# Kernel optimization log

Hardware: AMD Instinct MI355X
Metric: run time of the kernel (lower is better)

The kernel has to match this reference:

```python
import jax, jax.numpy as jnp
import numpy as np

N, G, E, H, Z = 50000, 2000, 800000, 512, 64
BN_EPS = 1e-5


def setup_inputs() -> dict:
    key = jax.random.key(0)
    ks = jax.random.split(key, 10)
    x = jax.random.normal(ks[0], (N, G), dtype=jnp.float32)
    edge_index = jax.random.randint(ks[1], (2, E), 0, N, dtype=jnp.int32)
    s1 = 1.0 / np.sqrt(G)
    s2 = 1.0 / np.sqrt(H)
    return {
        "x": x,
        "edge_index": edge_index,
        "W1l": jax.random.normal(ks[2], (G, H), dtype=jnp.float32) * s1,
        "b1": jnp.zeros((H,), jnp.float32),
        "W1r": jax.random.normal(ks[3], (G, H), dtype=jnp.float32) * s1,
        "bn_gamma": jax.random.uniform(ks[4], (H,), dtype=jnp.float32) + 0.5,
        "bn_beta": jax.random.normal(ks[5], (H,), dtype=jnp.float32) * 0.1,
        "bn_mean": jax.random.normal(ks[6], (H,), dtype=jnp.float32) * 0.1,
        "bn_var": jax.random.uniform(ks[7], (H,), dtype=jnp.float32) + 0.5,
        "W2l": jax.random.normal(ks[8], (H, Z), dtype=jnp.float32) * s2,
        "b2": jnp.zeros((Z,), jnp.float32),
        "W2r": jax.random.normal(ks[9], (H, Z), dtype=jnp.float32) * s2,
    }


def _sage_conv(h, src, dst, Wl, bl, Wr, n_nodes):
    # mean aggregation of source features at destination nodes
    msg = h[src]  # [E, D] gather
    agg = jax.ops.segment_sum(msg, dst, num_segments=n_nodes)
    cnt = jax.ops.segment_sum(jnp.ones((src.shape[0],), h.dtype), dst, num_segments=n_nodes)
    agg = agg / jnp.maximum(cnt, 1.0)[:, None]
    # PyG SAGEConv: lin_l(agg) + lin_r(x), bias only on lin_l
    return agg @ Wl + bl + h @ Wr


def reference(x, edge_index, W1l, b1, W1r, bn_gamma, bn_beta, bn_mean, bn_var, W2l, b2, W2r):
    src, dst = edge_index[0], edge_index[1]
    n = x.shape[0]
    h = _sage_conv(x, src, dst, W1l, b1, W1r, n)  # [N, H]
    # BatchNorm1d (eval mode: running stats) + ReLU; dropout is identity at inference
    h = (h - bn_mean) * (bn_gamma / jnp.sqrt(bn_var + BN_EPS)) + bn_beta
    h = jax.nn.relu(h)
    z = _sage_conv(h, src, dst, W2l, b2, W2r, n)  # [N, Z]
    return z
```

## Files before the change

kernel.cpp:

```cpp
#include <hip/hip_runtime.h>


#define BN_EPS 1e-5f
#define GK 2000
#define KP 2048
#define NKT 32
#define NT2 16

typedef __attribute__((ext_vector_type(8))) short bf16x8;
typedef __attribute__((ext_vector_type(4))) float f32x4;
typedef unsigned short u16x8 __attribute__((ext_vector_type(8)));

__device__ inline unsigned short f2bf(float f) {
    union { float f; unsigned u; } v; v.f = f;
    unsigned r = (v.u + 0x7fffu + ((v.u >> 16) & 1u)) >> 16;
    return (unsigned short)r;
}
__device__ inline float bf2f(unsigned short u) {
    union { unsigned u; float f; } v; v.u = ((unsigned)u) << 16;
    return v.f;
}

#define GLL16(gp, lp) __builtin_amdgcn_global_load_lds( \
    (const __attribute__((address_space(1))) void*)(gp), \
    (__attribute__((address_space(3))) void*)(lp), 16, 0, 0)

__global__ __launch_bounds__(256) void prep_fused(
    const float* __restrict__ W1l, const float* __restrict__ W1r,
    const float* __restrict__ gamma, const float* __restrict__ beta,
    const float* __restrict__ mean, const float* __restrict__ var,
    const float* __restrict__ b1, unsigned short* __restrict__ BT,
    const float* __restrict__ W2l, const float* __restrict__ W2r,
    unsigned short* __restrict__ BT2, float* __restrict__ b1p,
    const int* __restrict__ ei, int* __restrict__ cnt, int E)
{
    const int bb = blockIdx.x;
    if (bb < 1024) {
        int idx = bb * 256 + threadIdx.x;
        int c  = idx >> 8;
        int k0 = (idx & 255) << 3;
        int cc = (c < 512) ? c : c - 512;
        float scv = gamma[cc] * rsqrtf(var[cc] + BN_EPS);
        const float* W = (c < 512) ? (W1l + cc) : (W1r + cc);
        unsigned short us[8];
#pragma unroll
        for (int j = 0; j < 8; ++j) {
            int k = k0 + j;
            float v = (k < GK) ? W[(size_t)k * 512] * scv : 0.0f;
            us[j] = f2bf(v);
        }
        *(u16x8*)&BT[(size_t)c * KP + k0] = *(u16x8*)us;
    } else if (bb < 1056) {
        int idx = (bb - 1024) * 256 + threadIdx.x;
        int c  = idx >> 6;
        int k0 = (idx & 63) << 3;
        const float* W = (c < 64) ? (W2l + c) : (W2r + (c - 64));
        unsigned short us[8];
#pragma unroll
        for (int j = 0; j < 8; ++j) us[j] = f2bf(W[(size_t)(k0 + j) * 64]);
        *(u16x8*)&BT2[(size_t)c * 512 + k0] = *(u16x8*)us;
    } else if (bb == 1056) {
#pragma unroll
        for (int h = 0; h < 2; ++h) {
            int c = threadIdx.x + h * 256;
            float scv = gamma[c] * rsqrtf(var[c] + BN_EPS);
            b1p[c] = b1[c] * scv + (beta[c] - mean[c] * scv);
        }
    } else {
        for (int i = (bb - 1057) * 256 + threadIdx.x; i < E; i += 1024 * 256)
            atomicAdd(&cnt[ei[E + i]], 1);
    }
}

__global__ __launch_bounds__(1024) void scan_kernel(const int* __restrict__ cnt,
                                                    int* __restrict__ row_start, int n) {
    __shared__ int part[1024];
    int t = threadIdx.x;
    int chunk = (n + 1023) >> 10;
    int lo = t * chunk;
    int hi = lo + chunk; if (hi > n) hi = n;
    int s = 0;
    for (int i = lo; i < hi; ++i) s += cnt[i];
    part[t] = s;
    __syncthreads();
    for (int off = 1; off < 1024; off <<= 1) {
        int add = (t >= off) ? part[t - off] : 0;
        __syncthreads();
        part[t] += add;
        __syncthreads();
    }
    int run = (t == 0) ? 0 : part[t - 1];
    for (int i = lo; i < hi; ++i) { row_start[i] = run; run += cnt[i]; }
    if (t == 1023) row_start[n] = part[1023];
}

__global__ __launch_bounds__(256) void convfill_kernel(
    const float* __restrict__ x, unsigned short* __restrict__ xb, int N,
    const int* __restrict__ ei, int E, const int* __restrict__ row_start,
    int* __restrict__ cnt, int* __restrict__ colidx)
{
    const int bb = blockIdx.x;
    if (bb < 2048) {
        const int total8 = N * 256;
        for (int idx = bb * 256 + threadIdx.x; idx < total8; idx += 2048 * 256) {
            int row = idx >> 8;
            int k8  = idx & 255;
            unsigned short us[8];
            if (k8 < 250) {
                const float4* p = (const float4*)(x + (size_t)row * 2000 + k8 * 8);
                float4 v0 = p[0], v1 = p[1];
                us[0]=f2bf(v0.x); us[1]=f2bf(v0.y); us[2]=f2bf(v0.z); us[3]=f2bf(v0.w);
                us[4]=f2bf(v1.x); us[5]=f2bf(v1.y); us[6]=f2bf(v1.z); us[7]=f2bf(v1.w);
            } else {
#pragma unroll
                for (int j = 0; j < 8; ++j) us[j] = 0;
            }
            *(u16x8*)&xb[(size_t)row * 2048 + k8 * 8] = *(u16x8*)us;
        }
    } else {
        int i = (bb - 2048) * 256 + threadIdx.x;
        if (i < E) {
            int d = ei[E + i];
            int p = atomicSub(&cnt[d], 1) - 1;
            colidx[row_start[d] + p] = ei[i];
        }
    }
}

__global__ __launch_bounds__(512) void gemm1_256(
    const unsigned short* __restrict__ xb, int M,
    const unsigned short* __restrict__ BT,
    unsigned short* __restrict__ Y)
{
    __shared__ __align__(16) unsigned short As[2][16384];
    __shared__ __align__(16) unsigned short Bs[2][16384];

    const int t = threadIdx.x, wid = t >> 6, lane = t & 63;
    const int nbr = (M + 255) >> 8;
    const int nwg = nbr * 4;
    const int b   = blockIdx.x;
    int swz = ((nwg & 7) == 0) ? (b & 7) * (nwg >> 3) + (b >> 3) : b;
    const int row0 = (swz >> 2) << 8;
    const int col0 = (swz & 3) << 8;

    const unsigned short* aSrc[4];
    const unsigned short* bSrc[4];
#pragma unroll
    for (int j = 0; j < 4; ++j) {
        int c = t + 512 * j;
        int l = (c & 7) ^ ((c >> 3) & 7);
        int rA = row0 + (c >> 3); if (rA >= M) rA = M - 1;
        aSrc[j] = xb + (size_t)rA * KP + l * 8;
        bSrc[j] = BT + (size_t)(col0 + (c >> 3)) * KP + l * 8;
    }

#define STG_HA0(kt, buf) do { \
        GLL16(aSrc[0] + (size_t)(kt) * 64, &As[buf][(size_t)t * 8]); \
        GLL16(aSrc[1] + (size_t)(kt) * 64, &As[buf][(size_t)(t + 512) * 8]); } while (0)
#define STG_HA1(kt, buf) do { \
        GLL16(aSrc[2] + (size_t)(kt) * 64, &As[buf][(size_t)(1024 + t) * 8]); \
        GLL16(aSrc[3] + (size_t)(kt) * 64, &As[buf][(size_t)(1536 + t) * 8]); } while (0)
#define STG_HB0(kt, buf) do { \
        GLL16(bSrc[0] + (size_t)(kt) * 64, &Bs[buf][(size_t)t * 8]); \
        GLL16(bSrc[1] + (size_t)(kt) * 64, &Bs[buf][(size_t)(t + 512) * 8]); } while (0)
#define STG_HB1(kt, buf) do { \
        GLL16(bSrc[2] + (size_t)(kt) * 64, &Bs[buf][(size_t)(1024 + t) * 8]); \
        GLL16(bSrc[3] + (size_t)(kt) * 64, &Bs[buf][(size_t)(1536 + t) * 8]); } while (0)

    const int wr = wid >> 2, wc = wid & 3;
    const int fr16 = lane & 15;
    const int j4  = lane >> 4;
    const int sl7 = fr16 & 7;
    const int sA0 = ((j4    ) ^ sl7) << 4;
    const int sA1 = ((4 + j4) ^ sl7) << 4;
    const int rbA = (wr * 128 + fr16) << 7;
    const int rbB = (wc * 64  + fr16) << 7;

    f32x4 acc[8][4];
#pragma unroll
    for (int m = 0; m < 8; ++m)
#pragma unroll
        for (int n = 0; n < 4; ++n) acc[m][n] = (f32x4)0.0f;

    STG_HB0(0, 0); STG_HA0(0, 0); STG_HA1(0, 0); STG_HB1(0, 0);
    STG_HB0(1, 1); STG_HA0(1, 1); STG_HA1(1, 1);
    asm volatile("s_waitcnt vmcnt(6)" ::: "memory");
    __builtin_amdgcn_s_barrier();
    __builtin_amdgcn_sched_barrier(0);

    for (int tk = 0; tk < NKT; ++tk) {
        const int buf = tk & 1, obuf = buf ^ 1;
        const char* Ab = (const char*)&As[buf][0];
        const char* Bb = (const char*)&Bs[buf][0];
        bf16x8 af[4][2], bfA[2][2], bfB[2][2];

#pragma unroll
        for (int m = 0; m < 4; ++m) {
            af[m][0] = *(const bf16x8*)(Ab + rbA + (m << 11) + sA0);
            af[m][1] = *(const bf16x8*)(Ab + rbA + (m << 11) + sA1);
        }
#pragma unroll
        for (int n = 0; n < 2; ++n) {
            bfA[n][0] = *(const bf16x8*)(Bb + rbB + (n << 11) + sA0);
            bfA[n][1] = *(const bf16x8*)(Bb + rbB + (n << 11) + sA1);
        }
        STG_HB1(tk + 1, obuf);
        __builtin_amdgcn_s_barrier();
        __builtin_amdgcn_sched_barrier(0);
        __builtin_amdgcn_s_setprio(1);
#pragma unroll
        for (int m = 0; m < 4; ++m)
#pragma unroll
            for (int n = 0; n < 2; ++n) {
                acc[m][n] = __builtin_amdgcn_mfma_f32_16x16x32_bf16(
                    af[m][0], bfA[n][0], acc[m][n], 0, 0, 0);
                acc[m][n] = __builtin_amdgcn_mfma_f32_16x16x32_bf16(
                    af[m][1], bfA[n][1], acc[m][n], 0, 0, 0);
            }
        __builtin_amdgcn_s_setprio(0);

#pragma unroll
        for (int n = 0; n < 2; ++n) {
            bfB[n][0] = *(const bf16x8*)(Bb + rbB + ((n + 2) << 11) + sA0);
            bfB[n][1] = *(const bf16x8*)(Bb + rbB + ((n + 2) << 11) + sA1);
        }
        asm volatile("s_waitcnt lgkmcnt(0)" ::: "memory");
        __builtin_amdgcn_s_barrier();
        __builtin_amdgcn_sched_barrier(0);
        __builtin_amdgcn_s_setprio(1);
#pragma unroll
        for (int m = 0; m < 4; ++m)
#pragma unroll
            for (int n = 0; n < 2; ++n) {
                acc[m][n + 2] = __builtin_amdgcn_mfma_f32_16x16x32_bf16(
                    af[m][0], bfB[n][0], acc[m][n + 2], 0, 0, 0);
                acc[m][n + 2] = __builtin_amdgcn_mfma_f32_16x16x32_bf16(
                    af[m][1], bfB[n][1], acc[m][n + 2], 0, 0, 0);
            }
        __builtin_amdgcn_s_setprio(0);

#pragma unroll
        for (int m = 0; m < 4; ++m) {
            af[m][0] = *(const bf16x8*)(Ab + rbA + ((m + 4) << 11) + sA0);
            af[m][1] = *(const bf16x8*)(Ab + rbA + ((m + 4) << 11) + sA1);
        }
        STG_HB0(tk + 2, buf);
        asm volatile("s_waitcnt lgkmcnt(0)" ::: "memory");
        __builtin_amdgcn_s_barrier();
        __builtin_amdgcn_sched_barrier(0);
        __builtin_amdgcn_s_setprio(1);
#pragma unroll
        for (int m = 0; m < 4; ++m)
#pragma unroll
            for (int n = 0; n < 2; ++n) {
                acc[m + 4][n] = __builtin_amdgcn_mfma_f32_16x16x32_bf16(
                    af[m][0], bfA[n][0], acc[m + 4][n], 0, 0, 0);
                acc[m + 4][n] = __builtin_amdgcn_mfma_f32_16x16x32_bf16(
                    af[m][1], bfA[n][1], acc[m + 4][n], 0, 0, 0);
            }
        __builtin_amdgcn_s_setprio(0);

        STG_HA0(tk + 2, buf);
        STG_HA1(tk + 2, buf);
        asm volatile("s_waitcnt vmcnt(6)" ::: "memory");
        __builtin_amdgcn_s_barrier();
        __builtin_amdgcn_sched_barrier(0);
        __builtin_amdgcn_s_setprio(1);
#pragma unroll
        for (int m = 0; m < 4; ++m)
#pragma unroll
            for (int n = 0; n < 2; ++n) {
                acc[m + 4][n + 2] = __builtin_amdgcn_mfma_f32_16x16x32_bf16(
                    af[m][0], bfB[n][0], acc[m + 4][n + 2], 0, 0, 0);
                acc[m + 4][n + 2] = __builtin_amdgcn_mfma_f32_16x16x32_bf16(
                    af[m][1], bfB[n][1], acc[m + 4][n + 2], 0, 0, 0);
            }
        __builtin_amdgcn_s_setprio(0);
    }
#undef STG_HA0
#undef STG_HA1
#undef STG_HB0
#undef STG_HB1

    const int crow = (lane >> 4) << 2;
#pragma unroll
    for (int m = 0; m < 8; ++m) {
        int rbase = row0 + wr * 128 + m * 16 + crow;
#pragma unroll
        for (int r = 0; r < 4; ++r) {
            int row = rbase + r;
            if (row < M) {
                unsigned short* Yp = Y + (size_t)row * 1024 + col0 + wc * 64 + fr16;
#pragma unroll
                for (int n = 0; n < 4; ++n)
                    Yp[n * 16] = f2bf(acc[m][n][r]);
            }
        }
    }
}

__global__ __launch_bounds__(256) void agg1_kernel(
    const unsigned short* __restrict__ Y, unsigned short* __restrict__ Hh,
    const int* __restrict__ row_start, const int* __restrict__ colidx,
    const float* __restrict__ b1p, int n)
{
    int wid  = (blockIdx.x * blockDim.x + threadIdx.x) >> 6;
    int lane = threadIdx.x & 63;
    if (wid >= n) return;
    int c0 = lane * 8;
    float bb[8];
    *(float4*)&bb[0] = *(const float4*)&b1p[c0];
    *(float4*)&bb[4] = *(const float4*)&b1p[c0 + 4];

    int s0 = row_start[wid], s1 = row_start[wid + 1];
    float acc[8] = {0, 0, 0, 0, 0, 0, 0, 0};
    int i = s0;
    for (; i + 4 <= s1; i += 4) {
        int src0 = colidx[i], src1 = colidx[i + 1];
        int src2 = colidx[i + 2], src3 = colidx[i + 3];
        u16x8 v0 = *(const u16x8*)&Y[(size_t)src0 * 1024 + c0];
        u16x8 v1 = *(const u16x8*)&Y[(size_t)src1 * 1024 + c0];
        u16x8 v2 = *(const u16x8*)&Y[(size_t)src2 * 1024 + c0];
        u16x8 v3 = *(const u16x8*)&Y[(size_t)src3 * 1024 + c0];
#pragma unroll
        for (int j = 0; j < 8; ++j)
            acc[j] += (bf2f(v0[j]) + bf2f(v1[j])) + (bf2f(v2[j]) + bf2f(v3[j]));
    }
    for (; i < s1; ++i) {
        int src = colidx[i];
        u16x8 v = *(const u16x8*)&Y[(size_t)src * 1024 + c0];
#pragma unroll
        for (int j = 0; j < 8; ++j) acc[j] += bf2f(v[j]);
    }
    float inv = 1.0f / fmaxf((float)(s1 - s0), 1.0f);
    u16x8 sv = *(const u16x8*)&Y[(size_t)wid * 1024 + 512 + c0];
    unsigned short o[8];
#pragma unroll
    for (int j = 0; j < 8; ++j) {
        float pre = acc[j] * inv + bb[j] + bf2f(sv[j]);
        o[j] = f2bf(fmaxf(pre, 0.0f));
    }
    *(u16x8*)&Hh[(size_t)wid * 512 + c0] = *(u16x8*)o;
}

__global__ __launch_bounds__(256) void gemm2_bf16(
    const unsigned short* __restrict__ Hh, int M,
    const unsigned short* __restrict__ BT2,
    unsigned short* __restrict__ U)
{
    __shared__ __align__(16) unsigned short As2[2][128][32];
    __shared__ __align__(16) unsigned short Bs2[2][128][32];

    const int t    = threadIdx.x;
    const int wid  = t >> 6;
    const int lane = t & 63;
    const int row0 = blockIdx.x << 7;

    const int c_lo = wid * 64 + lane;
    const int c_hi = c_lo + 256;
    const int s_lo = ((c_lo & 3) ^ ((c_lo >> 3) & 3)) << 3;
    const int s_hi = ((c_hi & 3) ^ ((c_hi >> 3) & 3)) << 3;
    int ra = row0 + (c_lo >> 2); if (ra >= M) ra = M - 1;
    int rbw = row0 + (c_hi >> 2); if (rbw >= M) rbw = M - 1;
    const unsigned short* aSrc0 = Hh + (size_t)ra * 512 + s_lo;
    const unsigned short* aSrc1 = Hh + (size_t)rbw * 512 + s_hi;
    const unsigned short* bSrc0 = BT2 + (size_t)(c_lo >> 2) * 512 + s_lo;
    const unsigned short* bSrc1 = BT2 + (size_t)(c_hi >> 2) * 512 + s_hi;

    const int wr   = wid >> 1, wc = wid & 1;
    const int fr16 = lane & 15;
    const int gsw2 = ((lane >> 4) ^ ((fr16 >> 1) & 3)) << 4;

    f32x4 acc[4][4];
#pragma unroll
    for (int m = 0; m < 4; ++m)
#pragma unroll
        for (int n = 0; n < 4; ++n) acc[m][n] = (f32x4)0.0f;

#define STAGE2(kt, buf) do {                                                  \
        int ko = (kt) * 32;                                                   \
        GLL16(aSrc0 + ko, (unsigned short*)&As2[buf][0][0] + (size_t)c_lo * 8);  \
        GLL16(aSrc1 + ko, (unsigned short*)&As2[buf][0][0] + (size_t)c_hi * 8);  \
        GLL16(bSrc0 + ko, (unsigned short*)&Bs2[buf][0][0] + (size_t)c_lo * 8);  \
        GLL16(bSrc1 + ko, (unsigned short*)&Bs2[buf][0][0] + (size_t)c_hi * 8);  \
    } while (0)

    STAGE2(0, 0);
    int cur = 0;
    for (int it = 0; it < NT2; ++it) {
        __syncthreads();
        if (it + 1 < NT2) STAGE2(it + 1, cur ^ 1);

        const char* Ab = (const char*)&As2[cur][0][0];
        const char* Bb = (const char*)&Bs2[cur][0][0];
        bf16x8 af[4], bfr[4];
#pragma unroll
        for (int m = 0; m < 4; ++m)
            af[m] = *(const bf16x8*)(Ab + ((wr * 64 + m * 16 + fr16) << 6) + gsw2);
#pragma unroll
        for (int n = 0; n < 4; ++n)
            bfr[n] = *(const bf16x8*)(Bb + ((wc * 64 + n * 16 + fr16) << 6) + gsw2);
#pragma unroll
        for (int m = 0; m < 4; ++m)
#pragma unroll
            for (int n = 0; n < 4; ++n)
                acc[m][n] = __builtin_amdgcn_mfma_f32_16x16x32_bf16(
                    af[m], bfr[n], acc[m][n], 0, 0, 0);
        cur ^= 1;
    }
#undef STAGE2

    const int crow = (lane >> 4) << 2;
#pragma unroll
    for (int m = 0; m < 4; ++m) {
        int rbase = row0 + wr * 64 + m * 16 + crow;
#pragma unroll
        for (int r = 0; r < 4; ++r) {
            int row = rbase + r;
            if (row < M) {
                unsigned short* Up = U + (size_t)row * 128 + wc * 64 + fr16;
#pragma unroll
                for (int n = 0; n < 4; ++n)
                    Up[n * 16] = f2bf(acc[m][n][r]);
            }
        }
    }
}

__global__ __launch_bounds__(256) void agg2_kernel(
    const unsigned short* __restrict__ U,
    const int* __restrict__ row_start, const int* __restrict__ colidx,
    const float* __restrict__ b2, float* __restrict__ out, int n)
{
    int wid  = (blockIdx.x * blockDim.x + threadIdx.x) >> 6;
    int lane = threadIdx.x & 63;
    if (wid >= n) return;
    int s0 = row_start[wid], s1 = row_start[wid + 1];
    float acc = 0.f;
    int i = s0;
    for (; i + 4 <= s1; i += 4) {
        int src0 = colidx[i], src1 = colidx[i + 1];
        int src2 = colidx[i + 2], src3 = colidx[i + 3];
        acc += (bf2f(U[(size_t)src0 * 128 + lane]) + bf2f(U[(size_t)src1 * 128 + lane]))
             + (bf2f(U[(size_t)src2 * 128 + lane]) + bf2f(U[(size_t)src3 * 128 + lane]));
    }
    for (; i < s1; ++i) acc += bf2f(U[(size_t)colidx[i] * 128 + lane]);
    float inv = 1.0f / fmaxf((float)(s1 - s0), 1.0f);
    float z = acc * inv + b2[lane] + bf2f(U[(size_t)wid * 128 + 64 + lane]);
    out[(size_t)wid * 64 + lane] = z;
}

extern "C" void kernel_launch(void* const* d_in, const int* in_sizes, int n_in,
                              void* d_out, int out_size, void* d_ws, size_t ws_size,
                              hipStream_t stream) {
    const float* x     = (const float*)d_in[0];
    const int*   ei    = (const int*)d_in[1];
    const float* W1l   = (const float*)d_in[2];
    const float* b1    = (const float*)d_in[3];
    const float* W1r   = (const float*)d_in[4];
    const float* gamma = (const float*)d_in[5];
    const float* beta  = (const float*)d_in[6];
    const float* mean  = (const float*)d_in[7];
    const float* var   = (const float*)d_in[8];
    const float* W2l   = (const float*)d_in[9];
    const float* b2    = (const float*)d_in[10];
    const float* W2r   = (const float*)d_in[11];
    float* out = (float*)d_out;

    const int N = in_sizes[0] / 2000;
    const int E = in_sizes[1] / 2;
    const int nby = (N + 127) / 128;

    char* ws = (char*)d_ws;
    unsigned short* xb  = (unsigned short*)ws;
    unsigned short* Y   = xb + (size_t)N * KP;
    unsigned short* BT  = Y + (size_t)N * 1024;
    unsigned short* BT2 = BT + (size_t)1024 * KP;
    float* b1p     = (float*)(BT2 + (size_t)128 * 512);
    int* cnt       = (int*)(b1p + 512);
    int* row_start = cnt + N;
    int* colidx    = row_start + N + 4;
    unsigned short* Hh = xb;
    unsigned short* U  = Y;

    hipMemsetAsync(cnt, 0, (size_t)N * sizeof(int), stream);

    prep_fused<<<2081, 256, 0, stream>>>(
        W1l, W1r, gamma, beta, mean, var, b1, BT, W2l, W2r, BT2, b1p,
        ei, cnt, E);

    scan_kernel<<<1, 1024, 0, stream>>>(cnt, row_start, N);

    int eb = (E + 255) / 256;
    convfill_kernel<<<2048 + eb, 256, 0, stream>>>(
        x, xb, N, ei, E, row_start, cnt, colidx);

    int nbr = (N + 255) / 256;
    gemm1_256<<<nbr * 4, 512, 0, stream>>>(xb, N, BT, Y);
    agg1_kernel<<<(N + 3) / 4, 256, 0, stream>>>(
        Y, Hh, row_start, colidx, b1p, N);
    gemm2_bf16<<<nby, 256, 0, stream>>>(Hh, N, BT2, U);
    agg2_kernel<<<(N + 3) / 4, 256, 0, stream>>>(
        U, row_start, colidx, b2, out, N);
}
```

Baseline: 681.1 us.

## Move x bf16 conversion into prep kernel and CSR fill into GEMM1 launch

The x-to-bf16 conversion now runs inside the prep kernel alongside the weight packing and degree counting. The CSR column fill runs as extra tail blocks of the GEMM1 launch. Together this removes the separate convfill kernel launch. The fill blocks still declare the GEMM's large shared memory, and the x conversion now sits in front of the scan rather than after it.

```diff
diff --git a/kernel.cpp b/kernel.cpp
--- a/kernel.cpp
+++ b/kernel.cpp
@@ -25,7 +25,8 @@
     (const __attribute__((address_space(1))) void*)(gp), \
     (__attribute__((address_space(3))) void*)(lp), 16, 0, 0)
 
-__global__ __launch_bounds__(256) void prep_fused(
+__global__ __launch_bounds__(256) void prep2(
+    const float* __restrict__ x, unsigned short* __restrict__ xb, int N,
     const float* __restrict__ W1l, const float* __restrict__ W1r,
     const float* __restrict__ gamma, const float* __restrict__ beta,
     const float* __restrict__ mean, const float* __restrict__ var,
@@ -35,8 +36,25 @@
     const int* __restrict__ ei, int* __restrict__ cnt, int E)
 {
     const int bb = blockIdx.x;
-    if (bb < 1024) {
-        int idx = bb * 256 + threadIdx.x;
+    if (bb < 2048) {
+        const int total8 = N * 256;
+        for (int idx = bb * 256 + threadIdx.x; idx < total8; idx += 2048 * 256) {
+            int row = idx >> 8;
+            int k8  = idx & 255;
+            unsigned short us[8];
+            if (k8 < 250) {
+                const float4* p = (const float4*)(x + (size_t)row * 2000 + k8 * 8);
+                float4 v0 = p[0], v1 = p[1];
+                us[0]=f2bf(v0.x); us[1]=f2bf(v0.y); us[2]=f2bf(v0.z); us[3]=f2bf(v0.w);
+                us[4]=f2bf(v1.x); us[5]=f2bf(v1.y); us[6]=f2bf(v1.z); us[7]=f2bf(v1.w);
+            } else {
+#pragma unroll
+                for (int j = 0; j < 8; ++j) us[j] = 0;
+            }
+            *(u16x8*)&xb[(size_t)row * 2048 + k8 * 8] = *(u16x8*)us;
+        }
+    } else if (bb < 3072) {
+        int idx = (bb - 2048) * 256 + threadIdx.x;
         int c  = idx >> 8;
         int k0 = (idx & 255) << 3;
         int cc = (c < 512) ? c : c - 512;
@@ -50,8 +68,8 @@
             us[j] = f2bf(v);
         }
         *(u16x8*)&BT[(size_t)c * KP + k0] = *(u16x8*)us;
-    } else if (bb < 1056) {
-        int idx = (bb - 1024) * 256 + threadIdx.x;
+    } else if (bb < 3104) {
+        int idx = (bb - 3072) * 256 + threadIdx.x;
         int c  = idx >> 6;
         int k0 = (idx & 63) << 3;
         const float* W = (c < 64) ? (W2l + c) : (W2r + (c - 64));
@@ -59,7 +77,7 @@
 #pragma unroll
         for (int j = 0; j < 8; ++j) us[j] = f2bf(W[(size_t)(k0 + j) * 64]);
         *(u16x8*)&BT2[(size_t)c * 512 + k0] = *(u16x8*)us;
-    } else if (bb == 1056) {
+    } else if (bb == 3104) {
 #pragma unroll
         for (int h = 0; h < 2; ++h) {
             int c = threadIdx.x + h * 256;
@@ -67,7 +85,7 @@
             b1p[c] = b1[c] * scv + (beta[c] - mean[c] * scv);
         }
     } else {
-        for (int i = (bb - 1057) * 256 + threadIdx.x; i < E; i += 1024 * 256)
+        for (int i = (bb - 3105) * 256 + threadIdx.x; i < E; i += 1024 * 256)
             atomicAdd(&cnt[ei[E + i]], 1);
     }
 }
@@ -94,51 +112,32 @@
     if (t == 1023) row_start[n] = part[1023];
 }
 
-__global__ __launch_bounds__(256) void convfill_kernel(
-    const float* __restrict__ x, unsigned short* __restrict__ xb, int N,
+__global__ __launch_bounds__(512) void gemm1_256(
+    const unsigned short* __restrict__ xb, int M,
+    const unsigned short* __restrict__ BT,
+    unsigned short* __restrict__ Y,
     const int* __restrict__ ei, int E, const int* __restrict__ row_start,
     int* __restrict__ cnt, int* __restrict__ colidx)
 {
-    const int bb = blockIdx.x;
-    if (bb < 2048) {
-        const int total8 = N * 256;
-        for (int idx = bb * 256 + threadIdx.x; idx < total8; idx += 2048 * 256) {
-            int row = idx >> 8;
-            int k8  = idx & 255;
-            unsigned short us[8];
-            if (k8 < 250) {
-                const float4* p = (const float4*)(x + (size_t)row * 2000 + k8 * 8);
-                float4 v0 = p[0], v1 = p[1];
-                us[0]=f2bf(v0.x); us[1]=f2bf(v0.y); us[2]=f2bf(v0.z); us[3]=f2bf(v0.w);
-                us[4]=f2bf(v1.x); us[5]=f2bf(v1.y); us[6]=f2bf(v1.z); us[7]=f2bf(v1.w);
-            } else {
-#pragma unroll
-                for (int j = 0; j < 8; ++j) us[j] = 0;
-            }
-            *(u16x8*)&xb[(size_t)row * 2048 + k8 * 8] = *(u16x8*)us;
-        }
-    } else {
-        int i = (bb - 2048) * 256 + threadIdx.x;
+    __shared__ __align__(16) unsigned short As[2][16384];
+    __shared__ __align__(16) unsigned short Bs[2][16384];
+
+    const int t = threadIdx.x;
+    const int nbr = (M + 255) >> 8;
+    const int nwg = nbr * 4;
+    const int b   = blockIdx.x;
+
+    if (b >= nwg) {
+        int i = (b - nwg) * 512 + t;
         if (i < E) {
             int d = ei[E + i];
             int p = atomicSub(&cnt[d], 1) - 1;
             colidx[row_start[d] + p] = ei[i];
         }
-    }
-}
-
-__global__ __launch_bounds__(512) void gemm1_256(
-    const unsigned short* __restrict__ xb, int M,
-    const unsigned short* __restrict__ BT,
-    unsigned short* __restrict__ Y)
-{
-    __shared__ __align__(16) unsigned short As[2][16384];
-    __shared__ __align__(16) unsigned short Bs[2][16384];
-
-    const int t = threadIdx.x, wid = t >> 6, lane = t & 63;
-    const int nbr = (M + 255) >> 8;
-    const int nwg = nbr * 4;
-    const int b   = blockIdx.x;
+        return;
+    }
+
+    const int wid = t >> 6, lane = t & 63;
     int swz = ((nwg & 7) == 0) ? (b & 7) * (nwg >> 3) + (b >> 3) : b;
     const int row0 = (swz >> 2) << 8;
     const int col0 = (swz & 3) << 8;
@@ -485,18 +484,18 @@
 
     hipMemsetAsync(cnt, 0, (size_t)N * sizeof(int), stream);
 
-    prep_fused<<<2081, 256, 0, stream>>>(
-        W1l, W1r, gamma, beta, mean, var, b1, BT, W2l, W2r, BT2, b1p,
-        ei, cnt, E);
+    prep2<<<4129, 256, 0, stream>>>(
+        x, xb, N, W1l, W1r, gamma, beta, mean, var, b1, BT,
+        W2l, W2r, BT2, b1p, ei, cnt, E);
 
     scan_kernel<<<1, 1024, 0, stream>>>(cnt, row_start, N);
 
-    int eb = (E + 255) / 256;
-    convfill_kernel<<<2048 + eb, 256, 0, stream>>>(
-        x, xb, N, ei, E, row_start, cnt, colidx);
-
     int nbr = (N + 255) / 256;
-    gemm1_256<<<nbr * 4, 512, 0, stream>>>(xb, N, BT, Y);
+    int nwg = nbr * 4;
+    int fillb = (E + 511) / 512;
+    gemm1_256<<<nwg + fillb, 512, 0, stream>>>(
+        xb, N, BT, Y, ei, E, row_start, cnt, colidx);
+
     agg1_kernel<<<(N + 3) / 4, 256, 0, stream>>>(
         Y, Hh, row_start, colidx, b1p, N);
     gemm2_bf16<<<nby, 256, 0, stream>>>(Hh, N, BT2, U);
```

After: 654.9 us, median of 2. -3.8%, faster.
